# Performance work log

Measured on AMD Instinct MI355X. Metric: run time of the kernel, lower is better.

Reference implementation:

```python
import jax, jax.numpy as jnp
import numpy as np

BS, T, H = 4, 2048, 512
N_HEAD = 8
D_HEAD = H // N_HEAD  # 64


def setup_inputs() -> dict:
    key = jax.random.key(0)
    k1, k2, k3 = jax.random.split(key, 3)
    x = jax.random.normal(k1, (BS, T, H), dtype=jnp.float32)
    # torch Linear(hidden, (2*n_head+1)*d_head) -> store transposed for x @ W
    w_qkv = jax.random.normal(k2, (H, (2 * N_HEAD + 1) * D_HEAD), dtype=jnp.float32) * (H ** -0.5)
    w_out = jax.random.normal(k3, (D_HEAD, H), dtype=jnp.float32) * (D_HEAD ** -0.5)
    return {"x": x, "w_qkv": w_qkv, "w_out": w_out}


def reference(x, w_qkv, w_out):
    bs, t, h = x.shape
    n_head, d_head = N_HEAD, D_HEAD
    scale = d_head ** -0.5

    qkv = x @ w_qkv  # [bs, t, (2*n_head+1)*d_head]
    q, k, v = jnp.split(qkv, [n_head * d_head, 2 * n_head * d_head], axis=-1)
    q = q.reshape(bs, t, n_head, d_head)
    k = k.reshape(bs, t, n_head, d_head)
    # v stays [bs, t, d_head]: a single V shared across all heads

    # causal mask: -inf strictly above the diagonal
    mask = jnp.triu(jnp.full((t, t), -jnp.inf, dtype=x.dtype), 1)

    # scores: [bs, n_head, t_q, t_k]
    attn_score = jnp.einsum('bqhd,bkhd->bhqk', q, k) * scale + mask
    attn_prob = jax.nn.softmax(attn_score, axis=-1)

    # shared V broadcast over heads: [bs, n_head, t, d_head]
    attn_vec = jnp.einsum('bhqk,bkd->bhqd', attn_prob, v)
    m_attn_vec = jnp.mean(attn_vec, axis=1)  # mean over heads -> [bs, t, d_head]

    out = m_attn_vec @ w_out  # [bs, t, hidden]
    return out, attn_prob
```

## Files before the change

### kernel.cpp

```cpp
#include <hip/hip_runtime.h>

typedef unsigned short u16;
typedef __bf16 bf16x8 __attribute__((ext_vector_type(8)));
typedef float f32x4 __attribute__((ext_vector_type(4)));
static_assert(sizeof(bf16x8) == 16, "bf16x8 must be 16B");

#define MFMA(a, b, c) __builtin_amdgcn_mfma_f32_16x16x32_bf16(a, b, c, 0, 0, 0)

__device__ __forceinline__ u16 f2bf(float f) {
  unsigned u = __float_as_uint(f);
  u += 0x7fffu + ((u >> 16) & 1u);
  return (u16)(u >> 16);
}

__global__ __launch_bounds__(256) void prep_kernel(
    const float* __restrict__ x, const float* __restrict__ wqkv,
    const float* __restrict__ wout, u16* __restrict__ xh,
    u16* __restrict__ wt, u16* __restrict__ wot) {
  int blk = blockIdx.x, tid = threadIdx.x;
  if (blk < 4096) {
    int idx = (blk * 256 + tid) * 4;
    float4 v = *(const float4*)(x + idx);
    ushort4 o;
    o.x = f2bf(v.x); o.y = f2bf(v.y); o.z = f2bf(v.z); o.w = f2bf(v.w);
    *(ushort4*)(xh + idx) = o;
  } else if (blk < 4096 + 2176) {
    int idx = (blk - 4096) * 256 + tid;
    int n = idx >> 9, k = idx & 511;
    float v = wqkv[k * 1088 + n];
    if (n < 512) v *= 0.125f;
    wt[idx] = f2bf(v);
  } else {
    int idx = (blk - 6272) * 256 + tid;
    int n = idx >> 6, d = idx & 63;
    wot[idx] = f2bf(wout[d * 512 + n]);
  }
}

__global__ __launch_bounds__(256) void qkv_gemm_kernel(
    const u16* __restrict__ xh, const u16* __restrict__ wt,
    u16* __restrict__ Qb, u16* __restrict__ Kb, u16* __restrict__ Vt) {
  __shared__ u16 As[128][40];
  __shared__ u16 Bs[64][40];
  const int tid = threadIdx.x;
  const int w = tid >> 6, l = tid & 63, g = l >> 4, c16 = l & 15;
  const int n0 = blockIdx.x * 64;
  const int m0 = blockIdx.y * 128;
  const int arow = tid >> 1, acol = (tid & 1) << 4;
  const int brow = tid >> 2, bcol = (tid & 3) << 3;
  const u16* ap = xh + (size_t)(m0 + arow) * 512 + acol;
  const u16* bp = wt + (size_t)(n0 + brow) * 512 + bcol;
  uint4 pa0 = *(const uint4*)(ap);
  uint4 pa1 = *(const uint4*)(ap + 8);
  uint4 pb0 = *(const uint4*)(bp);
  f32x4 acc[2][4] = {};
  for (int k0 = 0; k0 < 512; k0 += 32) {
    __syncthreads();
    *(uint4*)&As[arow][acol] = pa0;
    *(uint4*)&As[arow][acol + 8] = pa1;
    *(uint4*)&Bs[brow][bcol] = pb0;
    __syncthreads();
    if (k0 + 32 < 512) {
      pa0 = *(const uint4*)(ap + k0 + 32);
      pa1 = *(const uint4*)(ap + k0 + 40);
      pb0 = *(const uint4*)(bp + k0 + 32);
    }
#pragma unroll
    for (int mt = 0; mt < 2; ++mt) {
      bf16x8 a = *(const bf16x8*)&As[w * 32 + mt * 16 + c16][g * 8];
#pragma unroll
      for (int nt = 0; nt < 4; ++nt) {
        bf16x8 b = *(const bf16x8*)&Bs[nt * 16 + c16][g * 8];
        acc[mt][nt] = MFMA(a, b, acc[mt][nt]);
      }
    }
  }
#pragma unroll
  for (int mt = 0; mt < 2; ++mt)
#pragma unroll
    for (int nt = 0; nt < 4; ++nt)
#pragma unroll
      for (int j = 0; j < 4; ++j) {
        u16 bv = f2bf(acc[mt][nt][j]);
        int row = m0 + w * 32 + mt * 16 + g * 4 + j;
        int b = row >> 11, t = row & 2047;
        int col = n0 + nt * 16 + c16;
        if (col < 512) {
          int h = col >> 6, d = col & 63;
          Qb[((size_t)((b << 3) + h) * 2048 + t) * 64 + d] = bv;
        } else if (col < 1024) {
          int cc = col - 512, h = cc >> 6, d = cc & 63;
          Kb[((size_t)((b << 3) + h) * 2048 + t) * 64 + d] = bv;
        } else {
          int d = col - 1024;
          Vt[((size_t)((b << 6) + d)) * 2048 + t] = bv;
        }
      }
}

__global__ __launch_bounds__(256) void attn_kernel(
    const u16* __restrict__ Qb, const u16* __restrict__ Kb,
    const u16* __restrict__ Vt, float* __restrict__ P,
    float* __restrict__ Obuf) {
  __shared__ u16 QP[64][72];
  __shared__ u16 Ks[64][72];
  __shared__ u16 Vs[64][72];
  const int tid = threadIdx.x;
  const int w = tid >> 6, l = tid & 63, g = l >> 4, c16 = l & 15;
  const int bidx = blockIdx.x;
  const int qt = bidx & 31, bh = bidx >> 5, b = bh >> 3;
  const int srow = tid >> 2, scol = (tid & 3) << 4;

  {
    const u16* src = Qb + ((size_t)(bh * 2048 + qt * 64 + srow)) * 64 + scol;
    *(uint4*)&QP[srow][scol] = *(const uint4*)(src);
    *(uint4*)&QP[srow][scol + 8] = *(const uint4*)(src + 8);
  }
  __syncthreads();
  const bf16x8 aq0 = *(const bf16x8*)&QP[w * 16 + c16][g * 8];
  const bf16x8 aq1 = *(const bf16x8*)&QP[w * 16 + c16][32 + g * 8];

  const u16* kbase = Kb + ((size_t)bh * 2048) * 64;
  const u16* vbase = Vt + ((size_t)(b << 6)) * 2048;

  float lsum[4] = {0.f, 0.f, 0.f, 0.f};

  uint4 ka0 = *(const uint4*)(kbase + (size_t)srow * 64 + scol);
  uint4 ka1 = *(const uint4*)(kbase + (size_t)srow * 64 + scol + 8);
  for (int kt = 0; kt <= qt; ++kt) {
    __syncthreads();
    *(uint4*)&Ks[srow][scol] = ka0;
    *(uint4*)&Ks[srow][scol + 8] = ka1;
    __syncthreads();
    if (kt < qt) {
      const u16* knext = kbase + (size_t)((kt + 1) * 64 + srow) * 64 + scol;
      ka0 = *(const uint4*)(knext);
      ka1 = *(const uint4*)(knext + 8);
    }
    float s[4][4];
#pragma unroll
    for (int nt = 0; nt < 4; ++nt) {
      bf16x8 bk0 = *(const bf16x8*)&Ks[nt * 16 + c16][g * 8];
      bf16x8 bk1 = *(const bf16x8*)&Ks[nt * 16 + c16][32 + g * 8];
      f32x4 a = {};
      a = MFMA(aq0, bk0, a);
      a = MFMA(aq1, bk1, a);
#pragma unroll
      for (int j = 0; j < 4; ++j) s[nt][j] = a[j];
    }
    if (kt == qt) {
#pragma unroll
      for (int nt = 0; nt < 4; ++nt)
#pragma unroll
        for (int j = 0; j < 4; ++j)
          if (nt * 16 + c16 > w * 16 + g * 4 + j) s[nt][j] = -3.0e38f;
    }
#pragma unroll
    for (int j = 0; j < 4; ++j)
      lsum[j] += __expf(s[0][j]) + __expf(s[1][j]) +
                 __expf(s[2][j]) + __expf(s[3][j]);
  }
  float rl[4];
#pragma unroll
  for (int j = 0; j < 4; ++j) {
#pragma unroll
    for (int dd = 1; dd < 16; dd <<= 1)
      lsum[j] += __shfl_xor(lsum[j], dd, 64);
    rl[j] = 1.0f / lsum[j];
  }

  f32x4 oacc[4] = {};
  ka0 = *(const uint4*)(kbase + (size_t)srow * 64 + scol);
  ka1 = *(const uint4*)(kbase + (size_t)srow * 64 + scol + 8);
  uint4 va0 = *(const uint4*)(vbase + (size_t)srow * 2048 + scol);
  uint4 va1 = *(const uint4*)(vbase + (size_t)srow * 2048 + scol + 8);
  for (int kt = 0; kt <= qt; ++kt) {
    __syncthreads();
    *(uint4*)&Ks[srow][scol] = ka0;
    *(uint4*)&Ks[srow][scol + 8] = ka1;
    *(uint4*)&Vs[srow][scol] = va0;
    *(uint4*)&Vs[srow][scol + 8] = va1;
    __syncthreads();
    if (kt < qt) {
      const u16* knext = kbase + (size_t)((kt + 1) * 64 + srow) * 64 + scol;
      ka0 = *(const uint4*)(knext);
      ka1 = *(const uint4*)(knext + 8);
      const u16* vnext = vbase + (size_t)srow * 2048 + (kt + 1) * 64 + scol;
      va0 = *(const uint4*)(vnext);
      va1 = *(const uint4*)(vnext + 8);
    }
    float s[4][4];
#pragma unroll
    for (int nt = 0; nt < 4; ++nt) {
      bf16x8 bk0 = *(const bf16x8*)&Ks[nt * 16 + c16][g * 8];
      bf16x8 bk1 = *(const bf16x8*)&Ks[nt * 16 + c16][32 + g * 8];
      f32x4 a = {};
      a = MFMA(aq0, bk0, a);
      a = MFMA(aq1, bk1, a);
#pragma unroll
      for (int j = 0; j < 4; ++j) s[nt][j] = a[j];
    }
    if (kt == qt) {
#pragma unroll
      for (int nt = 0; nt < 4; ++nt)
#pragma unroll
        for (int j = 0; j < 4; ++j)
          if (nt * 16 + c16 > w * 16 + g * 4 + j) s[nt][j] = -3.0e38f;
    }
    float* prow =
        P + ((size_t)(bh * 2048 + qt * 64 + w * 16)) * 2048 + (size_t)kt * 64;
#pragma unroll
    for (int nt = 0; nt < 4; ++nt)
#pragma unroll
      for (int j = 0; j < 4; ++j) {
        float p = __expf(s[nt][j]) * rl[j];
        __builtin_nontemporal_store(
            p, prow + (size_t)(g * 4 + j) * 2048 + nt * 16 + c16);
        QP[w * 16 + g * 4 + j][nt * 16 + c16] = f2bf(p);
      }
    bf16x8 ap0 = *(const bf16x8*)&QP[w * 16 + c16][g * 8];
    bf16x8 ap1 = *(const bf16x8*)&QP[w * 16 + c16][32 + g * 8];
#pragma unroll
    for (int nt = 0; nt < 4; ++nt) {
      bf16x8 bv0 = *(const bf16x8*)&Vs[nt * 16 + c16][g * 8];
      bf16x8 bv1 = *(const bf16x8*)&Vs[nt * 16 + c16][32 + g * 8];
      oacc[nt] = MFMA(ap0, bv0, oacc[nt]);
      oacc[nt] = MFMA(ap1, bv1, oacc[nt]);
    }
  }

  {
    float* obase = Obuf + ((size_t)(bh * 2048 + qt * 64 + w * 16)) * 64;
#pragma unroll
    for (int nt = 0; nt < 4; ++nt)
#pragma unroll
      for (int j = 0; j < 4; ++j)
        obase[(g * 4 + j) * 64 + nt * 16 + c16] = oacc[nt][j];
  }
  {
    int colstart = (qt + 1) * 64;
    int nf4 = (2048 - colstart) >> 2;
    float* base = P + ((size_t)(bh * 2048 + qt * 64)) * 2048;
    f32x4 z = {0.f, 0.f, 0.f, 0.f};
    for (int r = 0; r < 64; ++r) {
      f32x4* rowp = (f32x4*)(base + (size_t)r * 2048 + colstart);
      for (int u = tid; u < nf4; u += 256)
        __builtin_nontemporal_store(z, rowp + u);
    }
  }
}

__global__ __launch_bounds__(256) void mean_kernel(
    const float* __restrict__ Obuf, u16* __restrict__ meanb) {
  int o4 = blockIdx.x * 256 + threadIdx.x;
  int d4 = o4 & 15, t = (o4 >> 4) & 2047, b = o4 >> 15;
  f32x4 acc = {0.f, 0.f, 0.f, 0.f};
#pragma unroll
  for (int h = 0; h < 8; ++h) {
    f32x4 v = *(const f32x4*)(Obuf +
        ((size_t)((b << 3) + h) * 2048 + t) * 64 + d4 * 4);
    acc += v;
  }
  ushort4 o;
  o.x = f2bf(acc[0] * 0.125f); o.y = f2bf(acc[1] * 0.125f);
  o.z = f2bf(acc[2] * 0.125f); o.w = f2bf(acc[3] * 0.125f);
  *(ushort4*)(meanb + (size_t)o4 * 4) = o;
}

__global__ __launch_bounds__(256) void out_gemm_kernel(
    const u16* __restrict__ meanb, const u16* __restrict__ wot,
    float* __restrict__ out) {
  __shared__ u16 As[64][72];
  __shared__ u16 Bs[64][72];
  const int tid = threadIdx.x;
  const int w = tid >> 6, l = tid & 63, g = l >> 4, c16 = l & 15;
  const int n0 = blockIdx.x * 64;
  const int m0 = blockIdx.y * 64;
  const int srow = tid >> 2, scol = (tid & 3) << 4;
  {
    const u16* asrc = meanb + (size_t)(m0 + srow) * 64 + scol;
    *(uint4*)&As[srow][scol] = *(const uint4*)(asrc);
    *(uint4*)&As[srow][scol + 8] = *(const uint4*)(asrc + 8);
    const u16* bsrc = wot + (size_t)(n0 + srow) * 64 + scol;
    *(uint4*)&Bs[srow][scol] = *(const uint4*)(bsrc);
    *(uint4*)&Bs[srow][scol + 8] = *(const uint4*)(bsrc + 8);
  }
  __syncthreads();
  bf16x8 a0 = *(const bf16x8*)&As[w * 16 + c16][g * 8];
  bf16x8 a1 = *(const bf16x8*)&As[w * 16 + c16][32 + g * 8];
  f32x4 acc[4] = {};
#pragma unroll
  for (int nt = 0; nt < 4; ++nt) {
    bf16x8 b0 = *(const bf16x8*)&Bs[nt * 16 + c16][g * 8];
    bf16x8 b1 = *(const bf16x8*)&Bs[nt * 16 + c16][32 + g * 8];
    acc[nt] = MFMA(a0, b0, acc[nt]);
    acc[nt] = MFMA(a1, b1, acc[nt]);
  }
#pragma unroll
  for (int nt = 0; nt < 4; ++nt)
#pragma unroll
    for (int j = 0; j < 4; ++j)
      __builtin_nontemporal_store(
          acc[nt][j],
          out + (size_t)(m0 + w * 16 + g * 4 + j) * 512 + n0 + nt * 16 + c16);
}

extern "C" void kernel_launch(void* const* d_in, const int* in_sizes, int n_in,
                              void* d_out, int out_size, void* d_ws,
                              size_t ws_size, hipStream_t stream) {
  (void)in_sizes; (void)n_in; (void)out_size; (void)ws_size;
  const float* x = (const float*)d_in[0];
  const float* wqkv = (const float*)d_in[1];
  const float* wout = (const float*)d_in[2];
  float* out = (float*)d_out;
  float* P = out + 4194304;

  u16* xh = (u16*)d_ws;
  u16* wt = xh + 4194304;
  u16* wot = wt + 557056;
  u16* Qb = wot + 32768;
  u16* Kb = Qb + 4194304;
  u16* Vt = Kb + 4194304;
  float* Obuf = (float*)(Vt + 524288);
  u16* meanb = xh;

  hipLaunchKernelGGL(prep_kernel, dim3(6400), dim3(256), 0, stream,
                     x, wqkv, wout, xh, wt, wot);
  hipLaunchKernelGGL(qkv_gemm_kernel, dim3(17, 64), dim3(256), 0, stream,
                     xh, wt, Qb, Kb, Vt);
  hipLaunchKernelGGL(attn_kernel, dim3(1024), dim3(256), 0, stream,
                     Qb, Kb, Vt, P, Obuf);
  hipLaunchKernelGGL(mean_kernel, dim3(512), dim3(256), 0, stream,
                     Obuf, meanb);
  hipLaunchKernelGGL(out_gemm_kernel, dim3(8, 128), dim3(256), 0, stream,
                     meanb, wot, out);
}
```

Measured before the change: 669.8 us.

## Transpose attention score tiles so P stores and P@V stay in registers

The attention kernel now computes S^T (K as the A operand, Q as the B operand), so each lane holds four consecutive key columns of one query row. That lets it write P as a vectorized 16-byte nontemporal store and feed probabilities straight into 16x16x16 MFMAs without the bf16 round trip through shared memory. Because each wave now covers a slice of keys rather than a slice of queries, the row sums are reduced across waves through shared memory, and the per-wave partial outputs are combined with LDS atomics before being written to Obuf. The trade-off is more accumulator registers (a 4x4 set of f32x4), extra LDS atomic traffic and extra barriers.

Result: slower. 712.0 us (+6.3%).

```diff
diff --git a/kernel.cpp b/kernel.cpp
--- a/kernel.cpp
+++ b/kernel.cpp
@@ -2,10 +2,12 @@
 
 typedef unsigned short u16;
 typedef __bf16 bf16x8 __attribute__((ext_vector_type(8)));
+typedef short s16x4 __attribute__((ext_vector_type(4)));
 typedef float f32x4 __attribute__((ext_vector_type(4)));
 static_assert(sizeof(bf16x8) == 16, "bf16x8 must be 16B");
 
-#define MFMA(a, b, c) __builtin_amdgcn_mfma_f32_16x16x32_bf16(a, b, c, 0, 0, 0)
+#define MFMA32(a, b, c) __builtin_amdgcn_mfma_f32_16x16x32_bf16(a, b, c, 0, 0, 0)
+#define MFMA16(a, b, c) __builtin_amdgcn_mfma_f32_16x16x16bf16_1k(a, b, c, 0, 0, 0)
 
 __device__ __forceinline__ u16 f2bf(float f) {
   unsigned u = __float_as_uint(f);
@@ -71,7 +73,7 @@
 #pragma unroll
       for (int nt = 0; nt < 4; ++nt) {
         bf16x8 b = *(const bf16x8*)&Bs[nt * 16 + c16][g * 8];
-        acc[mt][nt] = MFMA(a, b, acc[mt][nt]);
+        acc[mt][nt] = MFMA32(a, b, acc[mt][nt]);
       }
     }
   }
@@ -102,29 +104,36 @@
     const u16* __restrict__ Qb, const u16* __restrict__ Kb,
     const u16* __restrict__ Vt, float* __restrict__ P,
     float* __restrict__ Obuf) {
-  __shared__ u16 QP[64][72];
-  __shared__ u16 Ks[64][72];
-  __shared__ u16 Vs[64][72];
+  __shared__ __align__(16) char smem[27648];
+  __shared__ float Lred[256];
+  u16 (*Qs)[72] = (u16(*)[72])smem;
+  u16 (*Ks)[72] = (u16(*)[72])(smem + 9216);
+  u16 (*Vs)[72] = (u16(*)[72])(smem + 18432);
+  float* Osum = (float*)smem;
+
   const int tid = threadIdx.x;
   const int w = tid >> 6, l = tid & 63, g = l >> 4, c16 = l & 15;
-  const int bidx = blockIdx.x;
-  const int qt = bidx & 31, bh = bidx >> 5, b = bh >> 3;
+  const int qt = blockIdx.x & 31, bh = blockIdx.x >> 5, b = bh >> 3;
   const int srow = tid >> 2, scol = (tid & 3) << 4;
+  const int kl = w * 16 + g * 4;
 
   {
     const u16* src = Qb + ((size_t)(bh * 2048 + qt * 64 + srow)) * 64 + scol;
-    *(uint4*)&QP[srow][scol] = *(const uint4*)(src);
-    *(uint4*)&QP[srow][scol + 8] = *(const uint4*)(src + 8);
-  }
-  __syncthreads();
-  const bf16x8 aq0 = *(const bf16x8*)&QP[w * 16 + c16][g * 8];
-  const bf16x8 aq1 = *(const bf16x8*)&QP[w * 16 + c16][32 + g * 8];
-
-  const u16* kbase = Kb + ((size_t)bh * 2048) * 64;
-  const u16* vbase = Vt + ((size_t)(b << 6)) * 2048;
+    *(uint4*)&Qs[srow][scol] = *(const uint4*)src;
+    *(uint4*)&Qs[srow][scol + 8] = *(const uint4*)(src + 8);
+  }
+  __syncthreads();
+  bf16x8 bq[4][2];
+#pragma unroll
+  for (int nt = 0; nt < 4; ++nt) {
+    bq[nt][0] = *(const bf16x8*)&Qs[nt * 16 + c16][g * 8];
+    bq[nt][1] = *(const bf16x8*)&Qs[nt * 16 + c16][32 + g * 8];
+  }
+
+  const u16* kbase = Kb + (size_t)bh * 2048 * 64;
+  const u16* vbase = Vt + (size_t)(b << 6) * 2048;
 
   float lsum[4] = {0.f, 0.f, 0.f, 0.f};
-
   uint4 ka0 = *(const uint4*)(kbase + (size_t)srow * 64 + scol);
   uint4 ka1 = *(const uint4*)(kbase + (size_t)srow * 64 + scol + 8);
   for (int kt = 0; kt <= qt; ++kt) {
@@ -133,43 +142,46 @@
     *(uint4*)&Ks[srow][scol + 8] = ka1;
     __syncthreads();
     if (kt < qt) {
-      const u16* knext = kbase + (size_t)((kt + 1) * 64 + srow) * 64 + scol;
-      ka0 = *(const uint4*)(knext);
-      ka1 = *(const uint4*)(knext + 8);
-    }
-    float s[4][4];
+      const u16* kn = kbase + (size_t)((kt + 1) * 64 + srow) * 64 + scol;
+      ka0 = *(const uint4*)kn;
+      ka1 = *(const uint4*)(kn + 8);
+    }
+    bf16x8 ak0 = *(const bf16x8*)&Ks[w * 16 + c16][g * 8];
+    bf16x8 ak1 = *(const bf16x8*)&Ks[w * 16 + c16][32 + g * 8];
 #pragma unroll
     for (int nt = 0; nt < 4; ++nt) {
-      bf16x8 bk0 = *(const bf16x8*)&Ks[nt * 16 + c16][g * 8];
-      bf16x8 bk1 = *(const bf16x8*)&Ks[nt * 16 + c16][32 + g * 8];
-      f32x4 a = {};
-      a = MFMA(aq0, bk0, a);
-      a = MFMA(aq1, bk1, a);
-#pragma unroll
-      for (int j = 0; j < 4; ++j) s[nt][j] = a[j];
-    }
-    if (kt == qt) {
-#pragma unroll
-      for (int nt = 0; nt < 4; ++nt)
+      f32x4 s = {};
+      s = MFMA32(ak0, bq[nt][0], s);
+      s = MFMA32(ak1, bq[nt][1], s);
+      const int qcol = nt * 16 + c16;
+      if (kt == qt) {
 #pragma unroll
         for (int j = 0; j < 4; ++j)
-          if (nt * 16 + c16 > w * 16 + g * 4 + j) s[nt][j] = -3.0e38f;
-    }
-#pragma unroll
-    for (int j = 0; j < 4; ++j)
-      lsum[j] += __expf(s[0][j]) + __expf(s[1][j]) +
-                 __expf(s[2][j]) + __expf(s[3][j]);
-  }
+          lsum[nt] += (kl + j > qcol) ? 0.0f : __expf(s[j]);
+      } else {
+#pragma unroll
+        for (int j = 0; j < 4; ++j) lsum[nt] += __expf(s[j]);
+      }
+    }
+  }
+#pragma unroll
+  for (int nt = 0; nt < 4; ++nt) {
+    lsum[nt] += __shfl_xor(lsum[nt], 16, 64);
+    lsum[nt] += __shfl_xor(lsum[nt], 32, 64);
+  }
+  if (g == 0) {
+#pragma unroll
+    for (int nt = 0; nt < 4; ++nt) Lred[w * 64 + nt * 16 + c16] = lsum[nt];
+  }
+  __syncthreads();
   float rl[4];
 #pragma unroll
-  for (int j = 0; j < 4; ++j) {
-#pragma unroll
-    for (int dd = 1; dd < 16; dd <<= 1)
-      lsum[j] += __shfl_xor(lsum[j], dd, 64);
-    rl[j] = 1.0f / lsum[j];
-  }
-
-  f32x4 oacc[4] = {};
+  for (int nt = 0; nt < 4; ++nt) {
+    int q = nt * 16 + c16;
+    rl[nt] = 1.0f / (Lred[q] + Lred[64 + q] + Lred[128 + q] + Lred[192 + q]);
+  }
+
+  f32x4 oacc[4][4] = {};
   ka0 = *(const uint4*)(kbase + (size_t)srow * 64 + scol);
   ka1 = *(const uint4*)(kbase + (size_t)srow * 64 + scol + 8);
   uint4 va0 = *(const uint4*)(vbase + (size_t)srow * 2048 + scol);
@@ -182,60 +194,62 @@
     *(uint4*)&Vs[srow][scol + 8] = va1;
     __syncthreads();
     if (kt < qt) {
-      const u16* knext = kbase + (size_t)((kt + 1) * 64 + srow) * 64 + scol;
-      ka0 = *(const uint4*)(knext);
-      ka1 = *(const uint4*)(knext + 8);
-      const u16* vnext = vbase + (size_t)srow * 2048 + (kt + 1) * 64 + scol;
-      va0 = *(const uint4*)(vnext);
-      va1 = *(const uint4*)(vnext + 8);
-    }
-    float s[4][4];
+      const u16* kn = kbase + (size_t)((kt + 1) * 64 + srow) * 64 + scol;
+      ka0 = *(const uint4*)kn;
+      ka1 = *(const uint4*)(kn + 8);
+      const u16* vn = vbase + (size_t)srow * 2048 + (kt + 1) * 64 + scol;
+      va0 = *(const uint4*)vn;
+      va1 = *(const uint4*)(vn + 8);
+    }
+    bf16x8 ak0 = *(const bf16x8*)&Ks[w * 16 + c16][g * 8];
+    bf16x8 ak1 = *(const bf16x8*)&Ks[w * 16 + c16][32 + g * 8];
+    s16x4 bv[4];
+#pragma unroll
+    for (int dc = 0; dc < 4; ++dc)
+      bv[dc] = *(const s16x4*)&Vs[dc * 16 + c16][kl];
+    float* pb = P + ((size_t)(bh * 2048 + qt * 64)) * 2048 + (size_t)kt * 64 + kl;
 #pragma unroll
     for (int nt = 0; nt < 4; ++nt) {
-      bf16x8 bk0 = *(const bf16x8*)&Ks[nt * 16 + c16][g * 8];
-      bf16x8 bk1 = *(const bf16x8*)&Ks[nt * 16 + c16][32 + g * 8];
-      f32x4 a = {};
-      a = MFMA(aq0, bk0, a);
-      a = MFMA(aq1, bk1, a);
-#pragma unroll
-      for (int j = 0; j < 4; ++j) s[nt][j] = a[j];
-    }
-    if (kt == qt) {
-#pragma unroll
-      for (int nt = 0; nt < 4; ++nt)
-#pragma unroll
-        for (int j = 0; j < 4; ++j)
-          if (nt * 16 + c16 > w * 16 + g * 4 + j) s[nt][j] = -3.0e38f;
-    }
-    float* prow =
-        P + ((size_t)(bh * 2048 + qt * 64 + w * 16)) * 2048 + (size_t)kt * 64;
-#pragma unroll
-    for (int nt = 0; nt < 4; ++nt)
-#pragma unroll
-      for (int j = 0; j < 4; ++j) {
-        float p = __expf(s[nt][j]) * rl[j];
-        __builtin_nontemporal_store(
-            p, prow + (size_t)(g * 4 + j) * 2048 + nt * 16 + c16);
-        QP[w * 16 + g * 4 + j][nt * 16 + c16] = f2bf(p);
+      f32x4 s = {};
+      s = MFMA32(ak0, bq[nt][0], s);
+      s = MFMA32(ak1, bq[nt][1], s);
+      const int qcol = nt * 16 + c16;
+      float p0 = __expf(s[0]) * rl[nt], p1 = __expf(s[1]) * rl[nt];
+      float p2 = __expf(s[2]) * rl[nt], p3 = __expf(s[3]) * rl[nt];
+      if (kt == qt) {
+        p0 = (kl + 0 > qcol) ? 0.f : p0;
+        p1 = (kl + 1 > qcol) ? 0.f : p1;
+        p2 = (kl + 2 > qcol) ? 0.f : p2;
+        p3 = (kl + 3 > qcol) ? 0.f : p3;
       }
-    bf16x8 ap0 = *(const bf16x8*)&QP[w * 16 + c16][g * 8];
-    bf16x8 ap1 = *(const bf16x8*)&QP[w * 16 + c16][32 + g * 8];
-#pragma unroll
-    for (int nt = 0; nt < 4; ++nt) {
-      bf16x8 bv0 = *(const bf16x8*)&Vs[nt * 16 + c16][g * 8];
-      bf16x8 bv1 = *(const bf16x8*)&Vs[nt * 16 + c16][32 + g * 8];
-      oacc[nt] = MFMA(ap0, bv0, oacc[nt]);
-      oacc[nt] = MFMA(ap1, bv1, oacc[nt]);
-    }
-  }
-
+      f32x4 pv = {p0, p1, p2, p3};
+      __builtin_nontemporal_store(pv, (f32x4*)(pb + (size_t)qcol * 2048));
+      s16x4 ap = {(short)f2bf(p0), (short)f2bf(p1),
+                  (short)f2bf(p2), (short)f2bf(p3)};
+#pragma unroll
+      for (int dc = 0; dc < 4; ++dc)
+        oacc[nt][dc] = MFMA16(ap, bv[dc], oacc[nt][dc]);
+    }
+  }
+
+  __syncthreads();
+  for (int i = tid; i < 64 * 68; i += 256) Osum[i] = 0.0f;
+  __syncthreads();
+#pragma unroll
+  for (int nt = 0; nt < 4; ++nt)
+#pragma unroll
+    for (int dc = 0; dc < 4; ++dc)
+#pragma unroll
+      for (int j = 0; j < 4; ++j)
+        atomicAdd(&Osum[(nt * 16 + g * 4 + j) * 68 + dc * 16 + c16],
+                  oacc[nt][dc][j]);
+  __syncthreads();
   {
-    float* obase = Obuf + ((size_t)(bh * 2048 + qt * 64 + w * 16)) * 64;
-#pragma unroll
-    for (int nt = 0; nt < 4; ++nt)
-#pragma unroll
-      for (int j = 0; j < 4; ++j)
-        obase[(g * 4 + j) * 64 + nt * 16 + c16] = oacc[nt][j];
+    float* ob = Obuf + ((size_t)(bh * 2048 + qt * 64 + srow)) * 64;
+    const int oc = (tid & 3) << 4;
+#pragma unroll
+    for (int q4 = 0; q4 < 4; ++q4)
+      *(f32x4*)(ob + oc + q4 * 4) = *(const f32x4*)&Osum[srow * 68 + oc + q4 * 4];
   }
   {
     int colstart = (qt + 1) * 64;
@@ -293,8 +307,8 @@
   for (int nt = 0; nt < 4; ++nt) {
     bf16x8 b0 = *(const bf16x8*)&Bs[nt * 16 + c16][g * 8];
     bf16x8 b1 = *(const bf16x8*)&Bs[nt * 16 + c16][32 + g * 8];
-    acc[nt] = MFMA(a0, b0, acc[nt]);
-    acc[nt] = MFMA(a1, b1, acc[nt]);
+    acc[nt] = MFMA32(a0, b0, acc[nt]);
+    acc[nt] = MFMA32(a1, b1, acc[nt]);
   }
 #pragma unroll
   for (int nt = 0; nt < 4; ++nt)
```
